# Performance work log

Measured on AMD Instinct MI355X. Metric: run time of the kernel, lower is better.

## Reference

```python
import jax, jax.numpy as jnp
import numpy as np

NUM_HEADS = 32
NEG_INF = -1e9


def setup_inputs() -> dict:
    key = jax.random.key(0)
    ks = jax.random.split(key, 7)
    B, S, H = 8, 4, 4096
    hd = H // NUM_HEADS
    position = 4096
    max_seq = position + S  # 4100
    sc = H ** -0.5  # keep projection outputs O(1)
    return {
        "hidden_states": jax.random.normal(ks[0], (B, S, H), jnp.float32),
        "Wq": jax.random.normal(ks[1], (H, H), jnp.float32) * sc,
        "Wk": jax.random.normal(ks[2], (H, H), jnp.float32) * sc,
        "Wv": jax.random.normal(ks[3], (H, H), jnp.float32) * sc,
        "Wo": jax.random.normal(ks[4], (H, H), jnp.float32) * sc,
        "key_cache": jax.random.normal(ks[5], (B, NUM_HEADS, max_seq, hd), jnp.float32),
        "value_cache": jax.random.normal(ks[6], (B, NUM_HEADS, max_seq, hd), jnp.float32),
        "position": position,
    }


def reference(hidden_states, Wq, Wk, Wv, Wo, key_cache, value_cache, position):
    B, S, H = hidden_states.shape
    nh = NUM_HEADS
    hd = H // nh
    scale = hd ** -0.5

    def proj(x, W):  # nn.Linear: x @ W.T -> [B, nh, S, hd]
        return (x @ W.T).reshape(B, S, nh, hd).transpose(0, 2, 1, 3)

    q = proj(hidden_states, Wq)
    k = proj(hidden_states, Wk)
    v = proj(hidden_states, Wv)

    # KV-cache slice update (position is a static Python int)
    key_cache = jax.lax.dynamic_update_slice(key_cache, k, (0, 0, position, 0))
    value_cache = jax.lax.dynamic_update_slice(value_cache, v, (0, 0, position, 0))

    kv_len = position + S
    k_all = key_cache[:, :, :kv_len, :]   # [B, nh, kv_len, hd]
    v_all = value_cache[:, :, :kv_len, :]

    scores = jnp.einsum('bhsd,bhtd->bhst', q, k_all) * scale  # [B, nh, S, kv_len]
    # triu(ones(S, kv_len), diagonal=position+1): mask col t when t > position + s
    mask = jnp.arange(kv_len)[None, :] > (position + jnp.arange(S))[:, None]
    scores = jnp.where(mask, NEG_INF, scores)
    attn = jax.nn.softmax(scores, axis=-1)

    out = jnp.einsum('bhst,bhtd->bhsd', attn, v_all)
    out = out.transpose(0, 2, 1, 3).reshape(B, S, H)
    return out @ Wo.T
```

## Files before the change

### kernel.cpp

```cpp
#include <hip/hip_runtime.h>
#include <cstdint>

#define HDIM   4096
#define NHEADS 32
#define HDH    128
#define BB     8
#define SQ     4
#define MAXSEQ 4100
#define QSCALE 0.08838834764831845f

#define PKCH  64
#define PLSTR 68
#define KSPL  512

__device__ __forceinline__ void dot4(float& a, const float4& p, const float4& q) {
    a = fmaf(p.x, q.x, fmaf(p.y, q.y, fmaf(p.z, q.z, fmaf(p.w, q.w, a))));
}

__global__ __launch_bounds__(256) void proj_split(
    const float* __restrict__ X,
    const float* __restrict__ W0, const float* __restrict__ W1, const float* __restrict__ W2,
    float* __restrict__ P)
{
    __shared__ float Wt[128][PLSTR];
    __shared__ float Xt[32][PLSTR];
    const float* __restrict__ W = (blockIdx.z == 0) ? W0 : ((blockIdx.z == 1) ? W1 : W2);
    const int tid = threadIdx.x;
    const int c0 = blockIdx.x * 128;
    const int kbase = blockIdx.y * KSPL;
    const int cg = tid & 31;
    const int rg = tid >> 5;

    float acc[4][4];
    #pragma unroll
    for (int r = 0; r < 4; ++r)
        #pragma unroll
        for (int j = 0; j < 4; ++j) acc[r][j] = 0.f;

    for (int ch = 0; ch < KSPL; ch += PKCH) {
        const int k0 = kbase + ch;
        #pragma unroll
        for (int i = 0; i < 8; ++i) {
            int fidx = (i << 8) + tid;
            int row = fidx >> 4;
            int kq = (fidx & 15) << 2;
            *(float4*)&Wt[row][kq] = *(const float4*)&W[(size_t)(c0 + row) * HDIM + k0 + kq];
        }
        #pragma unroll
        for (int i = 0; i < 2; ++i) {
            int fidx = (i << 8) + tid;
            int row = fidx >> 4;
            int kq = (fidx & 15) << 2;
            *(float4*)&Xt[row][kq] = *(const float4*)&X[(size_t)row * HDIM + k0 + kq];
        }
        __syncthreads();
        #pragma unroll 4
        for (int k = 0; k < PKCH; k += 4) {
            float4 w0 = *(const float4*)&Wt[cg][k];
            float4 w1 = *(const float4*)&Wt[cg + 32][k];
            float4 w2 = *(const float4*)&Wt[cg + 64][k];
            float4 w3 = *(const float4*)&Wt[cg + 96][k];
            float4 x0 = *(const float4*)&Xt[rg * 4 + 0][k];
            float4 x1 = *(const float4*)&Xt[rg * 4 + 1][k];
            float4 x2 = *(const float4*)&Xt[rg * 4 + 2][k];
            float4 x3 = *(const float4*)&Xt[rg * 4 + 3][k];
            dot4(acc[0][0], x0, w0); dot4(acc[0][1], x0, w1); dot4(acc[0][2], x0, w2); dot4(acc[0][3], x0, w3);
            dot4(acc[1][0], x1, w0); dot4(acc[1][1], x1, w1); dot4(acc[1][2], x1, w2); dot4(acc[1][3], x1, w3);
            dot4(acc[2][0], x2, w0); dot4(acc[2][1], x2, w1); dot4(acc[2][2], x2, w2); dot4(acc[2][3], x2, w3);
            dot4(acc[3][0], x3, w0); dot4(acc[3][1], x3, w1); dot4(acc[3][2], x3, w2); dot4(acc[3][3], x3, w3);
        }
        __syncthreads();
    }

    float* __restrict__ Pp = P + (size_t)(blockIdx.z * gridDim.y + blockIdx.y) * 32 * HDIM;
    #pragma unroll
    for (int r = 0; r < 4; ++r)
        #pragma unroll
        for (int j = 0; j < 4; ++j)
            Pp[(size_t)(rg * 4 + r) * HDIM + c0 + j * 32 + cg] = acc[r][j];
}

__global__ __launch_bounds__(256) void reduce_out(
    const float* __restrict__ P, float* __restrict__ out)
{
    const int idx = blockIdx.x * 256 + threadIdx.x;
    float s = 0.f;
    #pragma unroll
    for (int i = 0; i < 8; ++i) s += P[(size_t)i * 131072 + idx];
    out[idx] = s;
}

__device__ __forceinline__ float tree_reduce4(float p0, float p1, float p2, float p3, int li) {
    float a = (li & 16) ? p1 : p0;
    float b = (li & 16) ? p0 : p1;
    a += __shfl_xor(b, 16);
    float c = (li & 16) ? p3 : p2;
    float d = (li & 16) ? p2 : p3;
    c += __shfl_xor(d, 16);
    float e = (li & 8) ? c : a;
    float f = (li & 8) ? a : c;
    e += __shfl_xor(f, 8);
    e += __shfl_xor(e, 4);
    e += __shfl_xor(e, 2);
    e += __shfl_xor(e, 1);
    return e;
}

__global__ __launch_bounds__(1024) void attn_kernel(
    const float* __restrict__ kc, const float* __restrict__ vc,
    const float* __restrict__ Pq, float* __restrict__ ow,
    const int* __restrict__ posp)
{
    __shared__ __align__(16) float sc[MAXSEQ * 4];
    __shared__ __align__(16) float o_part[16][SQ][HDH];
    __shared__ __align__(16) float qs_lds[SQ * HDH];
    __shared__ __align__(16) float ks_lds[SQ * HDH];
    __shared__ __align__(16) float vs_lds[SQ * HDH];
    __shared__ float wmax[16][4];
    __shared__ float l_part[16][4];
    __shared__ float m_fin[4], l_fin[4];

    const int bh = blockIdx.x;
    const int pos = *posp;
    const int kvlen = pos + SQ;
    const int pos_main = pos & ~31;
    const int tid = threadIdx.x;
    const int w = tid >> 6;
    const int lane = tid & 63;
    const int half = (lane >> 5) & 1;
    const int li = lane & 31;
    const int sg = ((li >> 3) & 1) * 2 + ((li >> 4) & 1);

    {
        const int b = bh >> 5, h = bh & 31;
        if (tid < 512) {
            const int s = tid >> 7, d = tid & 127;
            const size_t base = (size_t)(b * SQ + s) * HDIM + h * HDH + d;
            float a = 0.f;
            #pragma unroll
            for (int i = 0; i < 8; ++i) a += Pq[(size_t)i * 131072 + base];
            qs_lds[tid] = a * QSCALE;
        } else {
            const int u = tid - 512;
            const int s = u >> 7, d = u & 127;
            const size_t base = (size_t)(b * SQ + s) * HDIM + h * HDH + d;
            float ak = 0.f, av = 0.f;
            #pragma unroll
            for (int i = 0; i < 8; ++i) {
                ak += Pq[(size_t)(8 + i) * 131072 + base];
                av += Pq[(size_t)(16 + i) * 131072 + base];
            }
            ks_lds[u] = ak;
            vs_lds[u] = av;
        }
    }
    __syncthreads();

    const float4 q0 = *(const float4*)&qs_lds[0 * HDH + li * 4];
    const float4 q1 = *(const float4*)&qs_lds[1 * HDH + li * 4];
    const float4 q2 = *(const float4*)&qs_lds[2 * HDH + li * 4];
    const float4 q3 = *(const float4*)&qs_lds[3 * HDH + li * 4];

    const float* __restrict__ kbase = kc + (size_t)bh * MAXSEQ * HDH + li * 4;
    const float* __restrict__ vbase = vc + (size_t)bh * MAXSEQ * HDH + li * 4;

    float mloc = -1e30f;

    {
        const int t0 = 2 * w + half;
        if (t0 < pos_main) {
            float4 ka = *(const float4*)(kbase + (size_t)t0 * HDH);
            float4 kb;
            if (t0 + 32 < pos_main) kb = *(const float4*)(kbase + (size_t)(t0 + 32) * HDH);
            for (int t = t0; t < pos_main; t += 32) {
                float4 kn;
                if (t + 64 < pos_main) kn = *(const float4*)(kbase + (size_t)(t + 64) * HDH);
                float p0 = fmaf(q0.x, ka.x, fmaf(q0.y, ka.y, fmaf(q0.z, ka.z, q0.w * ka.w)));
                float p1 = fmaf(q1.x, ka.x, fmaf(q1.y, ka.y, fmaf(q1.z, ka.z, q1.w * ka.w)));
                float p2 = fmaf(q2.x, ka.x, fmaf(q2.y, ka.y, fmaf(q2.z, ka.z, q2.w * ka.w)));
                float p3 = fmaf(q3.x, ka.x, fmaf(q3.y, ka.y, fmaf(q3.z, ka.z, q3.w * ka.w)));
                float e = tree_reduce4(p0, p1, p2, p3, li);
                mloc = fmaxf(mloc, e);
                if ((li & 7) == 0) sc[t * 4 + sg] = e;
                ka = kb; kb = kn;
            }
        }
        for (int tt = pos_main + 2 * w + half; tt < kvlen; tt += 32) {
            float4 k4;
            if (tt < pos) k4 = *(const float4*)(kbase + (size_t)tt * HDH);
            else          k4 = *(const float4*)&ks_lds[(tt - pos) * HDH + li * 4];
            float p0 = fmaf(q0.x, k4.x, fmaf(q0.y, k4.y, fmaf(q0.z, k4.z, q0.w * k4.w)));
            float p1 = fmaf(q1.x, k4.x, fmaf(q1.y, k4.y, fmaf(q1.z, k4.z, q1.w * k4.w)));
            float p2 = fmaf(q2.x, k4.x, fmaf(q2.y, k4.y, fmaf(q2.z, k4.z, q2.w * k4.w)));
            float p3 = fmaf(q3.x, k4.x, fmaf(q3.y, k4.y, fmaf(q3.z, k4.z, q3.w * k4.w)));
            float e = tree_reduce4(p0, p1, p2, p3, li);
            if (tt > pos + sg) e = -1e9f;
            mloc = fmaxf(mloc, e);
            if ((li & 7) == 0) sc[tt * 4 + sg] = e;
        }
    }
    float mw = fmaxf(mloc, __shfl_xor(mloc, 32));
    if (lane < 32 && (li & 7) == 0) wmax[w][sg] = mw;
    __syncthreads();
    if (tid < 4) {
        float m = wmax[0][tid];
        #pragma unroll
        for (int i = 1; i < 16; ++i) m = fmaxf(m, wmax[i][tid]);
        m_fin[tid] = m;
    }
    __syncthreads();
    const float mf0 = m_fin[0], mf1 = m_fin[1], mf2 = m_fin[2], mf3 = m_fin[3];

    float lp0 = 0.f, lp1 = 0.f, lp2 = 0.f, lp3 = 0.f;
    for (int t = tid; t < kvlen; t += 1024) {
        float4 s4 = *(float4*)&sc[t * 4];
        s4.x = __expf(s4.x - mf0);
        s4.y = __expf(s4.y - mf1);
        s4.z = __expf(s4.z - mf2);
        s4.w = __expf(s4.w - mf3);
        *(float4*)&sc[t * 4] = s4;
        lp0 += s4.x; lp1 += s4.y; lp2 += s4.z; lp3 += s4.w;
    }
    #pragma unroll
    for (int off = 32; off; off >>= 1) {
        lp0 += __shfl_xor(lp0, off);
        lp1 += __shfl_xor(lp1, off);
        lp2 += __shfl_xor(lp2, off);
        lp3 += __shfl_xor(lp3, off);
    }
    if (lane == 0) { l_part[w][0] = lp0; l_part[w][1] = lp1; l_part[w][2] = lp2; l_part[w][3] = lp3; }
    __syncthreads();
    if (tid < 4) {
        float L = 0.f;
        #pragma unroll
        for (int i = 0; i < 16; ++i) L += l_part[i][tid];
        l_fin[tid] = L;
    }

    float4 o0 = {0,0,0,0}, o1 = {0,0,0,0}, o2 = {0,0,0,0}, o3 = {0,0,0,0};
    {
        const int t0 = 2 * w + half;
        if (t0 < pos_main) {
            float4 va = *(const float4*)(vbase + (size_t)t0 * HDH);
            float4 vb;
            if (t0 + 32 < pos_main) vb = *(const float4*)(vbase + (size_t)(t0 + 32) * HDH);
            for (int t = t0; t < pos_main; t += 32) {
                float4 vn;
                if (t + 64 < pos_main) vn = *(const float4*)(vbase + (size_t)(t + 64) * HDH);
                float4 e4 = *(float4*)&sc[t * 4];
                o0.x = fmaf(e4.x, va.x, o0.x); o0.y = fmaf(e4.x, va.y, o0.y);
                o0.z = fmaf(e4.x, va.z, o0.z); o0.w = fmaf(e4.x, va.w, o0.w);
                o1.x = fmaf(e4.y, va.x, o1.x); o1.y = fmaf(e4.y, va.y, o1.y);
                o1.z = fmaf(e4.y, va.z, o1.z); o1.w = fmaf(e4.y, va.w, o1.w);
                o2.x = fmaf(e4.z, va.x, o2.x); o2.y = fmaf(e4.z, va.y, o2.y);
                o2.z = fmaf(e4.z, va.z, o2.z); o2.w = fmaf(e4.z, va.w, o2.w);
                o3.x = fmaf(e4.w, va.x, o3.x); o3.y = fmaf(e4.w, va.y, o3.y);
                o3.z = fmaf(e4.w, va.z, o3.z); o3.w = fmaf(e4.w, va.w, o3.w);
                va = vb; vb = vn;
            }
        }
        for (int tt = pos_main + 2 * w + half; tt < kvlen; tt += 32) {
            float4 v4;
            if (tt < pos) v4 = *(const float4*)(vbase + (size_t)tt * HDH);
            else          v4 = *(const float4*)&vs_lds[(tt - pos) * HDH + li * 4];
            float4 e4 = *(float4*)&sc[tt * 4];
            o0.x = fmaf(e4.x, v4.x, o0.x); o0.y = fmaf(e4.x, v4.y, o0.y);
            o0.z = fmaf(e4.x, v4.z, o0.z); o0.w = fmaf(e4.x, v4.w, o0.w);
            o1.x = fmaf(e4.y, v4.x, o1.x); o1.y = fmaf(e4.y, v4.y, o1.y);
            o1.z = fmaf(e4.y, v4.z, o1.z); o1.w = fmaf(e4.y, v4.w, o1.w);
            o2.x = fmaf(e4.z, v4.x, o2.x); o2.y = fmaf(e4.z, v4.y, o2.y);
            o2.z = fmaf(e4.z, v4.z, o2.z); o2.w = fmaf(e4.z, v4.w, o2.w);
            o3.x = fmaf(e4.w, v4.x, o3.x); o3.y = fmaf(e4.w, v4.y, o3.y);
            o3.z = fmaf(e4.w, v4.z, o3.z); o3.w = fmaf(e4.w, v4.w, o3.w);
        }
    }
    o0.x += __shfl_xor(o0.x, 32); o0.y += __shfl_xor(o0.y, 32);
    o0.z += __shfl_xor(o0.z, 32); o0.w += __shfl_xor(o0.w, 32);
    o1.x += __shfl_xor(o1.x, 32); o1.y += __shfl_xor(o1.y, 32);
    o1.z += __shfl_xor(o1.z, 32); o1.w += __shfl_xor(o1.w, 32);
    o2.x += __shfl_xor(o2.x, 32); o2.y += __shfl_xor(o2.y, 32);
    o2.z += __shfl_xor(o2.z, 32); o2.w += __shfl_xor(o2.w, 32);
    o3.x += __shfl_xor(o3.x, 32); o3.y += __shfl_xor(o3.y, 32);
    o3.z += __shfl_xor(o3.z, 32); o3.w += __shfl_xor(o3.w, 32);
    if (half == 0) {
        *(float4*)&o_part[w][0][li * 4] = o0;
        *(float4*)&o_part[w][1][li * 4] = o1;
        *(float4*)&o_part[w][2][li * 4] = o2;
        *(float4*)&o_part[w][3][li * 4] = o3;
    }
    __syncthreads();
    if (tid < 512) {
        const int s = tid >> 7, d = tid & 127;
        float a = 0.f;
        #pragma unroll
        for (int i = 0; i < 16; ++i) a += o_part[i][s][d];
        const int b = bh >> 5, h = bh & 31;
        ow[((size_t)(b * SQ + s) << 12) + (h << 7) + d] = a / l_fin[s];
    }
}

extern "C" void kernel_launch(void* const* d_in, const int* in_sizes, int n_in,
                              void* d_out, int out_size, void* d_ws, size_t ws_size,
                              hipStream_t stream) {
    const float* hs = (const float*)d_in[0];
    const float* Wq = (const float*)d_in[1];
    const float* Wk = (const float*)d_in[2];
    const float* Wv = (const float*)d_in[3];
    const float* Wo = (const float*)d_in[4];
    const float* kc = (const float*)d_in[5];
    const float* vc = (const float*)d_in[6];
    const int*  pos = (const int*)d_in[7];
    float* out = (float*)d_out;

    float* ws = (float*)d_ws;
    float* ow = ws;
    float* Pq = ws + 131072;
    float* Po = ws + 3276800;

    proj_split<<<dim3(32, 8, 3), 256, 0, stream>>>(hs, Wq, Wk, Wv, Pq);
    attn_kernel<<<256, 1024, 0, stream>>>(kc, vc, Pq, ow, pos);
    proj_split<<<dim3(32, 8, 1), 256, 0, stream>>>(ow, Wo, Wo, Wo, Po);
    reduce_out<<<512, 256, 0, stream>>>(Po, out);
}
```

Measured before the change: 330.0 us.

## Split attention over KV tiles with single-pass flash-style softmax and combine kernel

Attention is split across four KV-range tiles per (batch, head), so the grid grows from 256 to 1024 blocks of 512 threads. Each block reads K and V together in one streaming pass, computing exp(score) and accumulating the weighted V and the softmax denominator on the fly, instead of separate score, max, exp and V passes with a large LDS score buffer. A new combine kernel sums the partial outputs and denominators across tiles and normalizes. The running-max subtraction is dropped, which relies on scores staying small enough that exp does not overflow.

```diff
diff --git a/kernel.cpp b/kernel.cpp
--- a/kernel.cpp
+++ b/kernel.cpp
@@ -7,6 +7,7 @@
 #define BB     8
 #define SQ     4
 #define MAXSEQ 4100
+#define NTILE  4
 #define QSCALE 0.08838834764831845f
 
 #define PKCH  64
@@ -106,174 +107,129 @@
     return e;
 }
 
-__global__ __launch_bounds__(1024) void attn_kernel(
+__global__ __launch_bounds__(512) void attn_flash(
     const float* __restrict__ kc, const float* __restrict__ vc,
-    const float* __restrict__ Pq, float* __restrict__ ow,
+    const float* __restrict__ Pq, float* __restrict__ po, float* __restrict__ pl,
     const int* __restrict__ posp)
 {
-    __shared__ __align__(16) float sc[MAXSEQ * 4];
-    __shared__ __align__(16) float o_part[16][SQ][HDH];
-    __shared__ __align__(16) float qs_lds[SQ * HDH];
-    __shared__ __align__(16) float ks_lds[SQ * HDH];
-    __shared__ __align__(16) float vs_lds[SQ * HDH];
-    __shared__ float wmax[16][4];
-    __shared__ float l_part[16][4];
-    __shared__ float m_fin[4], l_fin[4];
+    __shared__ __align__(16) float qs[SQ * HDH];
+    __shared__ __align__(16) float ks[SQ * HDH];
+    __shared__ __align__(16) float vs[SQ * HDH];
+    __shared__ __align__(16) float o_part[8][SQ][HDH];
+    __shared__ float l_part[8][SQ];
 
     const int bh = blockIdx.x;
+    const int tile = blockIdx.y;
     const int pos = *posp;
     const int kvlen = pos + SQ;
-    const int pos_main = pos & ~31;
+    const int T = (kvlen + NTILE - 1) / NTILE;
+    const int t_start = tile * T;
+    const int t_end = min(kvlen, t_start + T);
+    const int t_me = min(t_end, pos);
     const int tid = threadIdx.x;
     const int w = tid >> 6;
     const int lane = tid & 63;
     const int half = (lane >> 5) & 1;
     const int li = lane & 31;
-    const int sg = ((li >> 3) & 1) * 2 + ((li >> 4) & 1);
+    const int h32 = lane & 32;
+    const int hw = 2 * w + half;
 
     {
         const int b = bh >> 5, h = bh & 31;
-        if (tid < 512) {
-            const int s = tid >> 7, d = tid & 127;
-            const size_t base = (size_t)(b * SQ + s) * HDIM + h * HDH + d;
-            float a = 0.f;
-            #pragma unroll
-            for (int i = 0; i < 8; ++i) a += Pq[(size_t)i * 131072 + base];
-            qs_lds[tid] = a * QSCALE;
-        } else {
-            const int u = tid - 512;
-            const int s = u >> 7, d = u & 127;
-            const size_t base = (size_t)(b * SQ + s) * HDIM + h * HDH + d;
+        const int s = tid >> 7, d = tid & 127;
+        const size_t base = (size_t)(b * SQ + s) * HDIM + h * HDH + d;
+        float aq = 0.f;
+        #pragma unroll
+        for (int i = 0; i < 8; ++i) aq += Pq[(size_t)i * 131072 + base];
+        qs[tid] = aq * QSCALE;
+        if (t_end > pos) {
             float ak = 0.f, av = 0.f;
             #pragma unroll
             for (int i = 0; i < 8; ++i) {
                 ak += Pq[(size_t)(8 + i) * 131072 + base];
                 av += Pq[(size_t)(16 + i) * 131072 + base];
             }
-            ks_lds[u] = ak;
-            vs_lds[u] = av;
+            ks[tid] = ak;
+            vs[tid] = av;
         }
     }
     __syncthreads();
 
-    const float4 q0 = *(const float4*)&qs_lds[0 * HDH + li * 4];
-    const float4 q1 = *(const float4*)&qs_lds[1 * HDH + li * 4];
-    const float4 q2 = *(const float4*)&qs_lds[2 * HDH + li * 4];
-    const float4 q3 = *(const float4*)&qs_lds[3 * HDH + li * 4];
+    const float4 q0 = *(const float4*)&qs[0 * HDH + li * 4];
+    const float4 q1 = *(const float4*)&qs[1 * HDH + li * 4];
+    const float4 q2 = *(const float4*)&qs[2 * HDH + li * 4];
+    const float4 q3 = *(const float4*)&qs[3 * HDH + li * 4];
 
     const float* __restrict__ kbase = kc + (size_t)bh * MAXSEQ * HDH + li * 4;
     const float* __restrict__ vbase = vc + (size_t)bh * MAXSEQ * HDH + li * 4;
 
-    float mloc = -1e30f;
-
-    {
-        const int t0 = 2 * w + half;
-        if (t0 < pos_main) {
-            float4 ka = *(const float4*)(kbase + (size_t)t0 * HDH);
-            float4 kb;
-            if (t0 + 32 < pos_main) kb = *(const float4*)(kbase + (size_t)(t0 + 32) * HDH);
-            for (int t = t0; t < pos_main; t += 32) {
-                float4 kn;
-                if (t + 64 < pos_main) kn = *(const float4*)(kbase + (size_t)(t + 64) * HDH);
-                float p0 = fmaf(q0.x, ka.x, fmaf(q0.y, ka.y, fmaf(q0.z, ka.z, q0.w * ka.w)));
-                float p1 = fmaf(q1.x, ka.x, fmaf(q1.y, ka.y, fmaf(q1.z, ka.z, q1.w * ka.w)));
-                float p2 = fmaf(q2.x, ka.x, fmaf(q2.y, ka.y, fmaf(q2.z, ka.z, q2.w * ka.w)));
-                float p3 = fmaf(q3.x, ka.x, fmaf(q3.y, ka.y, fmaf(q3.z, ka.z, q3.w * ka.w)));
-                float e = tree_reduce4(p0, p1, p2, p3, li);
-                mloc = fmaxf(mloc, e);
-                if ((li & 7) == 0) sc[t * 4 + sg] = e;
-                ka = kb; kb = kn;
+    float4 o0 = {0,0,0,0}, o1 = {0,0,0,0}, o2 = {0,0,0,0}, o3 = {0,0,0,0};
+    float l0 = 0.f, l1 = 0.f, l2 = 0.f, l3 = 0.f;
+
+    const int t0 = t_start + hw;
+    const int nmain = (t_me > t0) ? ((t_me - t0 + 15) >> 4) : 0;
+
+    if (nmain > 0) {
+        float4 ka = *(const float4*)(kbase + (size_t)t0 * HDH);
+        float4 va = *(const float4*)(vbase + (size_t)t0 * HDH);
+        float4 kb, vb;
+        if (nmain > 1) {
+            kb = *(const float4*)(kbase + (size_t)(t0 + 16) * HDH);
+            vb = *(const float4*)(vbase + (size_t)(t0 + 16) * HDH);
+        }
+        int t = t0;
+        for (int it = 0; it < nmain; ++it, t += 16) {
+            float4 kn, vn;
+            if (it + 2 < nmain) {
+                kn = *(const float4*)(kbase + (size_t)(t + 32) * HDH);
+                vn = *(const float4*)(vbase + (size_t)(t + 32) * HDH);
             }
-        }
-        for (int tt = pos_main + 2 * w + half; tt < kvlen; tt += 32) {
-            float4 k4;
-            if (tt < pos) k4 = *(const float4*)(kbase + (size_t)tt * HDH);
-            else          k4 = *(const float4*)&ks_lds[(tt - pos) * HDH + li * 4];
-            float p0 = fmaf(q0.x, k4.x, fmaf(q0.y, k4.y, fmaf(q0.z, k4.z, q0.w * k4.w)));
-            float p1 = fmaf(q1.x, k4.x, fmaf(q1.y, k4.y, fmaf(q1.z, k4.z, q1.w * k4.w)));
-            float p2 = fmaf(q2.x, k4.x, fmaf(q2.y, k4.y, fmaf(q2.z, k4.z, q2.w * k4.w)));
-            float p3 = fmaf(q3.x, k4.x, fmaf(q3.y, k4.y, fmaf(q3.z, k4.z, q3.w * k4.w)));
+            float p0 = fmaf(q0.x, ka.x, fmaf(q0.y, ka.y, fmaf(q0.z, ka.z, q0.w * ka.w)));
+            float p1 = fmaf(q1.x, ka.x, fmaf(q1.y, ka.y, fmaf(q1.z, ka.z, q1.w * ka.w)));
+            float p2 = fmaf(q2.x, ka.x, fmaf(q2.y, ka.y, fmaf(q2.z, ka.z, q2.w * ka.w)));
+            float p3 = fmaf(q3.x, ka.x, fmaf(q3.y, ka.y, fmaf(q3.z, ka.z, q3.w * ka.w)));
             float e = tree_reduce4(p0, p1, p2, p3, li);
-            if (tt > pos + sg) e = -1e9f;
-            mloc = fmaxf(mloc, e);
-            if ((li & 7) == 0) sc[tt * 4 + sg] = e;
-        }
-    }
-    float mw = fmaxf(mloc, __shfl_xor(mloc, 32));
-    if (lane < 32 && (li & 7) == 0) wmax[w][sg] = mw;
-    __syncthreads();
-    if (tid < 4) {
-        float m = wmax[0][tid];
-        #pragma unroll
-        for (int i = 1; i < 16; ++i) m = fmaxf(m, wmax[i][tid]);
-        m_fin[tid] = m;
-    }
-    __syncthreads();
-    const float mf0 = m_fin[0], mf1 = m_fin[1], mf2 = m_fin[2], mf3 = m_fin[3];
-
-    float lp0 = 0.f, lp1 = 0.f, lp2 = 0.f, lp3 = 0.f;
-    for (int t = tid; t < kvlen; t += 1024) {
-        float4 s4 = *(float4*)&sc[t * 4];
-        s4.x = __expf(s4.x - mf0);
-        s4.y = __expf(s4.y - mf1);
-        s4.z = __expf(s4.z - mf2);
-        s4.w = __expf(s4.w - mf3);
-        *(float4*)&sc[t * 4] = s4;
-        lp0 += s4.x; lp1 += s4.y; lp2 += s4.z; lp3 += s4.w;
-    }
-    #pragma unroll
-    for (int off = 32; off; off >>= 1) {
-        lp0 += __shfl_xor(lp0, off);
-        lp1 += __shfl_xor(lp1, off);
-        lp2 += __shfl_xor(lp2, off);
-        lp3 += __shfl_xor(lp3, off);
-    }
-    if (lane == 0) { l_part[w][0] = lp0; l_part[w][1] = lp1; l_part[w][2] = lp2; l_part[w][3] = lp3; }
-    __syncthreads();
-    if (tid < 4) {
-        float L = 0.f;
-        #pragma unroll
-        for (int i = 0; i < 16; ++i) L += l_part[i][tid];
-        l_fin[tid] = L;
-    }
-
-    float4 o0 = {0,0,0,0}, o1 = {0,0,0,0}, o2 = {0,0,0,0}, o3 = {0,0,0,0};
-    {
-        const int t0 = 2 * w + half;
-        if (t0 < pos_main) {
-            float4 va = *(const float4*)(vbase + (size_t)t0 * HDH);
-            float4 vb;
-            if (t0 + 32 < pos_main) vb = *(const float4*)(vbase + (size_t)(t0 + 32) * HDH);
-            for (int t = t0; t < pos_main; t += 32) {
-                float4 vn;
-                if (t + 64 < pos_main) vn = *(const float4*)(vbase + (size_t)(t + 64) * HDH);
-                float4 e4 = *(float4*)&sc[t * 4];
-                o0.x = fmaf(e4.x, va.x, o0.x); o0.y = fmaf(e4.x, va.y, o0.y);
-                o0.z = fmaf(e4.x, va.z, o0.z); o0.w = fmaf(e4.x, va.w, o0.w);
-                o1.x = fmaf(e4.y, va.x, o1.x); o1.y = fmaf(e4.y, va.y, o1.y);
-                o1.z = fmaf(e4.y, va.z, o1.z); o1.w = fmaf(e4.y, va.w, o1.w);
-                o2.x = fmaf(e4.z, va.x, o2.x); o2.y = fmaf(e4.z, va.y, o2.y);
-                o2.z = fmaf(e4.z, va.z, o2.z); o2.w = fmaf(e4.z, va.w, o2.w);
-                o3.x = fmaf(e4.w, va.x, o3.x); o3.y = fmaf(e4.w, va.y, o3.y);
-                o3.z = fmaf(e4.w, va.z, o3.z); o3.w = fmaf(e4.w, va.w, o3.w);
-                va = vb; vb = vn;
-            }
-        }
-        for (int tt = pos_main + 2 * w + half; tt < kvlen; tt += 32) {
-            float4 v4;
-            if (tt < pos) v4 = *(const float4*)(vbase + (size_t)tt * HDH);
-            else          v4 = *(const float4*)&vs_lds[(tt - pos) * HDH + li * 4];
-            float4 e4 = *(float4*)&sc[tt * 4];
-            o0.x = fmaf(e4.x, v4.x, o0.x); o0.y = fmaf(e4.x, v4.y, o0.y);
-            o0.z = fmaf(e4.x, v4.z, o0.z); o0.w = fmaf(e4.x, v4.w, o0.w);
-            o1.x = fmaf(e4.y, v4.x, o1.x); o1.y = fmaf(e4.y, v4.y, o1.y);
-            o1.z = fmaf(e4.y, v4.z, o1.z); o1.w = fmaf(e4.y, v4.w, o1.w);
-            o2.x = fmaf(e4.z, v4.x, o2.x); o2.y = fmaf(e4.z, v4.y, o2.y);
-            o2.z = fmaf(e4.z, v4.z, o2.z); o2.w = fmaf(e4.z, v4.w, o2.w);
-            o3.x = fmaf(e4.w, v4.x, o3.x); o3.y = fmaf(e4.w, v4.y, o3.y);
-            o3.z = fmaf(e4.w, v4.z, o3.z); o3.w = fmaf(e4.w, v4.w, o3.w);
-        }
-    }
+            float e0 = __shfl(e, h32 + 0);
+            float e1 = __shfl(e, h32 + 16);
+            float e2 = __shfl(e, h32 + 8);
+            float e3 = __shfl(e, h32 + 24);
+            e0 = __expf(e0); e1 = __expf(e1); e2 = __expf(e2); e3 = __expf(e3);
+            l0 += e0; l1 += e1; l2 += e2; l3 += e3;
+            o0.x = fmaf(e0, va.x, o0.x); o0.y = fmaf(e0, va.y, o0.y);
+            o0.z = fmaf(e0, va.z, o0.z); o0.w = fmaf(e0, va.w, o0.w);
+            o1.x = fmaf(e1, va.x, o1.x); o1.y = fmaf(e1, va.y, o1.y);
+            o1.z = fmaf(e1, va.z, o1.z); o1.w = fmaf(e1, va.w, o1.w);
+            o2.x = fmaf(e2, va.x, o2.x); o2.y = fmaf(e2, va.y, o2.y);
+            o2.z = fmaf(e2, va.z, o2.z); o2.w = fmaf(e2, va.w, o2.w);
+            o3.x = fmaf(e3, va.x, o3.x); o3.y = fmaf(e3, va.y, o3.y);
+            o3.z = fmaf(e3, va.z, o3.z); o3.w = fmaf(e3, va.w, o3.w);
+            ka = kb; kb = kn; va = vb; vb = vn;
+        }
+    }
+
+    for (int tt = t0 + 16 * nmain; tt < t_end; tt += 16) {
+        float4 k4 = *(const float4*)&ks[(tt - pos) * HDH + li * 4];
+        float4 v4 = *(const float4*)&vs[(tt - pos) * HDH + li * 4];
+        float p0 = fmaf(q0.x, k4.x, fmaf(q0.y, k4.y, fmaf(q0.z, k4.z, q0.w * k4.w)));
+        float p1 = fmaf(q1.x, k4.x, fmaf(q1.y, k4.y, fmaf(q1.z, k4.z, q1.w * k4.w)));
+        float p2 = fmaf(q2.x, k4.x, fmaf(q2.y, k4.y, fmaf(q2.z, k4.z, q2.w * k4.w)));
+        float p3 = fmaf(q3.x, k4.x, fmaf(q3.y, k4.y, fmaf(q3.z, k4.z, q3.w * k4.w)));
+        float e = tree_reduce4(p0, p1, p2, p3, li);
+        float e0 = (tt > pos + 0) ? 0.f : __expf(__shfl(e, h32 + 0));
+        float e1 = (tt > pos + 1) ? 0.f : __expf(__shfl(e, h32 + 16));
+        float e2 = (tt > pos + 2) ? 0.f : __expf(__shfl(e, h32 + 8));
+        float e3 = (tt > pos + 3) ? 0.f : __expf(__shfl(e, h32 + 24));
+        l0 += e0; l1 += e1; l2 += e2; l3 += e3;
+        o0.x = fmaf(e0, v4.x, o0.x); o0.y = fmaf(e0, v4.y, o0.y);
+        o0.z = fmaf(e0, v4.z, o0.z); o0.w = fmaf(e0, v4.w, o0.w);
+        o1.x = fmaf(e1, v4.x, o1.x); o1.y = fmaf(e1, v4.y, o1.y);
+        o1.z = fmaf(e1, v4.z, o1.z); o1.w = fmaf(e1, v4.w, o1.w);
+        o2.x = fmaf(e2, v4.x, o2.x); o2.y = fmaf(e2, v4.y, o2.y);
+        o2.z = fmaf(e2, v4.z, o2.z); o2.w = fmaf(e2, v4.w, o2.w);
+        o3.x = fmaf(e3, v4.x, o3.x); o3.y = fmaf(e3, v4.y, o3.y);
+        o3.z = fmaf(e3, v4.z, o3.z); o3.w = fmaf(e3, v4.w, o3.w);
+    }
+
     o0.x += __shfl_xor(o0.x, 32); o0.y += __shfl_xor(o0.y, 32);
     o0.z += __shfl_xor(o0.z, 32); o0.w += __shfl_xor(o0.w, 32);
     o1.x += __shfl_xor(o1.x, 32); o1.y += __shfl_xor(o1.y, 32);
@@ -282,21 +238,44 @@
     o2.z += __shfl_xor(o2.z, 32); o2.w += __shfl_xor(o2.w, 32);
     o3.x += __shfl_xor(o3.x, 32); o3.y += __shfl_xor(o3.y, 32);
     o3.z += __shfl_xor(o3.z, 32); o3.w += __shfl_xor(o3.w, 32);
+    l0 += __shfl_xor(l0, 32); l1 += __shfl_xor(l1, 32);
+    l2 += __shfl_xor(l2, 32); l3 += __shfl_xor(l3, 32);
     if (half == 0) {
         *(float4*)&o_part[w][0][li * 4] = o0;
         *(float4*)&o_part[w][1][li * 4] = o1;
         *(float4*)&o_part[w][2][li * 4] = o2;
         *(float4*)&o_part[w][3][li * 4] = o3;
+        if (li == 0) { l_part[w][0] = l0; l_part[w][1] = l1; l_part[w][2] = l2; l_part[w][3] = l3; }
     }
     __syncthreads();
-    if (tid < 512) {
+    {
         const int s = tid >> 7, d = tid & 127;
         float a = 0.f;
         #pragma unroll
-        for (int i = 0; i < 16; ++i) a += o_part[i][s][d];
-        const int b = bh >> 5, h = bh & 31;
-        ow[((size_t)(b * SQ + s) << 12) + (h << 7) + d] = a / l_fin[s];
-    }
+        for (int i = 0; i < 8; ++i) a += o_part[i][s][d];
+        po[((size_t)(bh * NTILE + tile) * SQ + s) * HDH + d] = a;
+    }
+    if (tid < SQ) {
+        float L = 0.f;
+        #pragma unroll
+        for (int i = 0; i < 8; ++i) L += l_part[i][tid];
+        pl[(bh * NTILE + tile) * SQ + tid] = L;
+    }
+}
+
+__global__ __launch_bounds__(512) void attn_combine(
+    const float* __restrict__ po, const float* __restrict__ pl, float* __restrict__ ow)
+{
+    const int idx = blockIdx.x * 512 + threadIdx.x;
+    const int bh = idx >> 9, s = (idx >> 7) & 3, d = idx & 127;
+    float O = 0.f, L = 0.f;
+    #pragma unroll
+    for (int t = 0; t < NTILE; ++t) {
+        O += po[((size_t)(bh * NTILE + t) * SQ + s) * HDH + d];
+        L += pl[(bh * NTILE + t) * SQ + s];
+    }
+    const int b = bh >> 5, h = bh & 31;
+    ow[((size_t)(b * SQ + s) << 12) + (h << 7) + d] = O / L;
 }
 
 extern "C" void kernel_launch(void* const* d_in, const int* in_sizes, int n_in,
@@ -316,9 +295,12 @@
     float* ow = ws;
     float* Pq = ws + 131072;
     float* Po = ws + 3276800;
+    float* po = ws + 4325376;
+    float* pl = ws + 4849664;
 
     proj_split<<<dim3(32, 8, 3), 256, 0, stream>>>(hs, Wq, Wk, Wv, Pq);
-    attn_kernel<<<256, 1024, 0, stream>>>(kc, vc, Pq, ow, pos);
+    attn_flash<<<dim3(256, NTILE), 512, 0, stream>>>(kc, vc, Pq, po, pl, pos);
+    attn_combine<<<256, 512, 0, stream>>>(po, pl, ow);
     proj_split<<<dim3(32, 8, 1), 256, 0, stream>>>(ow, Wo, Wo, Wo, Po);
     reduce_out<<<512, 256, 0, stream>>>(Po, out);
 }
```

Measured after the change: 302.6 us. 1.09x faster.
